# Optimization experiments

Hardware: AMD Instinct MI355X
Metric: run time of the kernel (lower is better)

## Reference

```python
import jax, jax.numpy as jnp
import numpy as np

HIDDEN = 512
HEADS = 8
DHEAD = HIDDEN // HEADS  # 64


def setup_inputs() -> dict:
    key = jax.random.key(0)
    ks = jax.random.split(key, 12)
    B, S = 2, 2048
    inp = {
        "q": jax.random.normal(ks[0], (B, S, HIDDEN), dtype=jnp.float32),
        "k": jax.random.normal(ks[1], (B, S, HIDDEN), dtype=jnp.float32),
        "v": jax.random.normal(ks[2], (B, S, HIDDEN), dtype=jnp.float32),
        "mask": jnp.zeros((B, 1, 1, S), dtype=bool),
    }
    scale = 1.0 / np.sqrt(HIDDEN)
    for i, name in enumerate(["Wq", "Wk", "Wv", "Wm"]):
        inp[name] = jax.random.normal(ks[3 + i], (HIDDEN, HIDDEN), dtype=jnp.float32) * scale
    for i, name in enumerate(["bq", "bk", "bv", "bm"]):
        inp[name] = jax.random.normal(ks[7 + i], (HIDDEN,), dtype=jnp.float32) * 0.01
    return inp


def reference(q, k, v, mask, Wq, Wk, Wv, Wm, bq, bk, bv, bm):
    B = q.shape[0]
    # Linear projections (torch Linear: x @ W.T + b)
    qh = (jnp.einsum("bsd,ed->bse", q, Wq) + bq).reshape(B, HEADS, -1, DHEAD)
    kh = (jnp.einsum("bsd,ed->bse", k, Wk) + bk).reshape(B, HEADS, -1, DHEAD)
    vh = (jnp.einsum("bsd,ed->bse", v, Wv) + bv).reshape(B, HEADS, -1, DHEAD)
    # NOTE: the original module reshapes [B,S,512] -> [B,8,S',64] directly
    # (splitting the sequence dim into heads, not the hidden dim); replicated here.
    s = jnp.einsum("bhqd,bhkd->bhqk", qh, kh) / jnp.sqrt(jnp.float32(DHEAD))
    s = jnp.where(mask, jnp.float32(-1e9), s)
    s = jax.nn.softmax(s, axis=-1)
    # dropout is identity in eval mode
    attn = jnp.einsum("bhqk,bhkd->bhqd", s, vh)  # [B,H,S',64]
    attn = attn.transpose(0, 2, 1, 3).reshape(B, -1, HIDDEN)
    return jnp.einsum("bsd,ed->bse", attn, Wm) + bm
```

## Files before the change

### kernel.cpp

```cpp
#include <hip/hip_runtime.h>
#include <hip/hip_bf16.h>
#include <math.h>

typedef float  f32x4 __attribute__((ext_vector_type(4)));
typedef short  s16x8 __attribute__((ext_vector_type(8)));
typedef short  s16x4 __attribute__((ext_vector_type(4)));
typedef unsigned short u16x4 __attribute__((ext_vector_type(4)));

__device__ inline unsigned short bfc(float f){
  __hip_bfloat16 h = __float2bfloat16(f);
  unsigned short u; __builtin_memcpy(&u, &h, 2); return u;
}

__device__ inline f32x4 mfma16(s16x4 a, s16x4 b, f32x4 c){
#if __has_builtin(__builtin_amdgcn_mfma_f32_16x16x16_bf16)
  return __builtin_amdgcn_mfma_f32_16x16x16_bf16(a, b, c, 0, 0, 0);
#elif __has_builtin(__builtin_amdgcn_mfma_f32_16x16x16bf16_1k)
  return __builtin_amdgcn_mfma_f32_16x16x16bf16_1k(a, b, c, 0, 0, 0);
#else
  asm("v_mfma_f32_16x16x16_bf16 %0, %1, %2, %0" : "+v"(c) : "v"(a), "v"(b));
  return c;
#endif
}

__device__ inline void gl_lds16(const unsigned short* g, unsigned short* l){
  __builtin_amdgcn_global_load_lds(
      (const __attribute__((address_space(1))) unsigned int*)g,
      (__attribute__((address_space(3))) unsigned int*)l, 16, 0, 0);
}

__global__ __launch_bounds__(256) void prep(const float* __restrict__ q, const float* __restrict__ k,
                                            const float* __restrict__ v,
                                            const float* __restrict__ w0, const float* __restrict__ w1,
                                            const float* __restrict__ w2, const float* __restrict__ w3,
                                            const unsigned char* __restrict__ mask,
                                            unsigned short* __restrict__ AP, unsigned short* __restrict__ WP,
                                            float* __restrict__ mf){
  int y = blockIdx.y;
  int t = blockIdx.x * 256 + threadIdx.x;
  if (y < 3){
    const float* src = y==0 ? q : (y==1 ? k : v);
    unsigned short* d = AP + (size_t)y * 2097152;
    int r = t >> 6, g = t & 63;
    const float* sp = src + (size_t)r * 512 + g * 8;
    f32x4 a0 = *(const f32x4*)sp;
    f32x4 a1 = *(const f32x4*)(sp + 4);
    s16x8 o = { (short)bfc(a0.x),(short)bfc(a0.y),(short)bfc(a0.z),(short)bfc(a0.w),
                (short)bfc(a1.x),(short)bfc(a1.y),(short)bfc(a1.z),(short)bfc(a1.w) };
    size_t off = ((size_t)(((r>>4)*16 + (g>>2))*64 + (g&3)*16 + (r&15))) * 8;
    *(s16x8*)(d + off) = o;
  } else if (y < 7){
    if (blockIdx.x < 128){
      int yy = y - 3;
      const float* src = yy==0 ? w0 : yy==1 ? w1 : yy==2 ? w2 : w3;
      int c = t >> 6, g = t & 63;
      const float* sp = src + (size_t)c * 512 + g * 8;
      f32x4 a0 = *(const f32x4*)sp;
      f32x4 a1 = *(const f32x4*)(sp + 4);
      s16x8 o = { (short)bfc(a0.x),(short)bfc(a0.y),(short)bfc(a0.z),(short)bfc(a0.w),
                  (short)bfc(a1.x),(short)bfc(a1.y),(short)bfc(a1.z),(short)bfc(a1.w) };
      size_t off = ((size_t)(((c>>4)*16 + (g>>2))*64 + (g&3)*16 + (c&15))) * 8;
      *(s16x8*)(WP + yy*262144 + off) = o;
    }
  } else if (t < 4096){
    mf[t] = mask[t] ? -1.442695e9f : 0.0f;
  }
}

__global__ __launch_bounds__(256) void proj_gemm(const unsigned short* __restrict__ Ap,
    const unsigned short* __restrict__ Wp,
    const float* __restrict__ bq, const float* __restrict__ bk, const float* __restrict__ bv,
    unsigned short* __restrict__ pout){
  int z = blockIdx.z;
  const unsigned short* A = Ap + (size_t)z * 2097152;
  const unsigned short* W = Wp + (size_t)z * 262144;
  const float* bias = z==0 ? bq : (z==1 ? bk : bv);
  unsigned short* out = pout + (size_t)z * 2097152;

  int w = threadIdx.x >> 6, lane = threadIdx.x & 63;
  int lr = lane & 15, lg = lane >> 4;
  int rt = blockIdx.x * 4 + w;
  int bn = blockIdx.y;

  f32x4 acc[4] = {};
  const unsigned short* Abase = A + ((size_t)rt*8192 + lane*8);
  const unsigned short* Wbase = W + ((size_t)bn*32768 + lane*8);
#pragma unroll 4
  for (int kc = 0; kc < 16; ++kc){
    s16x8 af = *(const s16x8*)(Abase + kc*512);
#pragma unroll
    for (int n = 0; n < 4; ++n){
      s16x8 bf = *(const s16x8*)(Wbase + ((size_t)n*16 + kc)*512);
      acc[n] = __builtin_amdgcn_mfma_f32_16x16x32_bf16(af, bf, acc[n], 0, 0, 0);
    }
  }
  int orow = rt*16 + lg*4;
#pragma unroll
  for (int n = 0; n < 4; ++n){
    int col = bn*64 + n*16 + lr;
    float bv_ = bias[col];
#pragma unroll
    for (int r = 0; r < 4; ++r)
      out[(size_t)(orow + r)*512 + col] = bfc(acc[n][r] + bv_);
  }
}

__global__ __launch_bounds__(256) void vtrans(const unsigned short* __restrict__ Pv,
                                              unsigned short* __restrict__ Vt){
  int kt = blockIdx.x, bh = blockIdx.y;
  int b = bh >> 3, h = bh & 7;
  __shared__ unsigned short t[64][65];
  const unsigned short* src = Pv + (size_t)(b*2048 + h*256)*512 + kt*4096;
  for (int i = threadIdx.x; i < 4096; i += 256){ int r = i >> 6, c = i & 63; t[r][c] = src[i]; }
  __syncthreads();
  unsigned short* dst = Vt + (size_t)bh*131072 + kt*64;
  for (int i = threadIdx.x; i < 4096; i += 256){ int d = i >> 6, kk = i & 63; dst[(size_t)d*2048 + kk] = t[kk][d]; }
}

__global__ __launch_bounds__(512, 4) void flash(const unsigned short* __restrict__ Pq,
                                             const unsigned short* __restrict__ Pk,
                                             const unsigned short* __restrict__ Vt,
                                             const float* __restrict__ mf,
                                             unsigned short* __restrict__ aout){
  int qt = blockIdx.x;
  int bh = blockIdx.y;
  int b = bh >> 3, h = bh & 7;
  int w = threadIdx.x >> 6;
  int wq = w & 1, wk = w >> 1;
  int lane = threadIdx.x & 63;
  int lr = lane & 15, lg = lane >> 4;

  const unsigned short* Qh  = Pq + (size_t)(b*2048 + h*256)*512;
  const unsigned short* Kh  = Pk + (size_t)(b*2048 + h*256)*512 + (size_t)wk*32768;
  const unsigned short* Vth = Vt + (size_t)bh*131072 + wk*512;
  const float* mp = mf + b*2048 + wk*512 + lg*4;

  __shared__ char smem[65536];
  unsigned short* ktile = (unsigned short*)smem;
  unsigned short* vtile = (unsigned short*)(smem + 32768);
  float* obuf = (float*)smem;
  float* mlb  = (float*)(smem + 49152);

  int krow_l = lane >> 3;
  int cxor  = (lane & 7) ^ krow_l;
  int kcol_l = cxor * 8;

  int vhalf32 = (cxor >> 2) * 32;
  int vkc = (cxor & 3) * 8;
  const unsigned short* kg0 = Kh + (size_t)(8*(wq*2+0) + krow_l)*64 + kcol_l;
  const unsigned short* kg1 = Kh + (size_t)(8*(wq*2+1) + krow_l)*64 + kcol_l;
  const unsigned short* vg0 = Vth + (size_t)(wq*16 + 0 + krow_l + vhalf32)*2048 + vkc;
  const unsigned short* vg1 = Vth + (size_t)(wq*16 + 8 + krow_l + vhalf32)*2048 + vkc;

  s16x8 qf[2][2];
#pragma unroll
  for (int qq = 0; qq < 2; ++qq){
    int qrow = qt*64 + wq*32 + qq*16 + lr;
    qf[qq][0] = *(const s16x8*)(Qh + (size_t)qrow*64 + lg*8);
    qf[qq][1] = *(const s16x8*)(Qh + (size_t)qrow*64 + 32 + lg*8);
  }

  float m2[2] = {-INFINITY, -INFINITY}, l[2] = {0.f, 0.f};
  f32x4 accT[2][4] = {};
  int kswz = (lr & 7) * 16;

#define STAGE(dbuf) { \
    unsigned short* kd = ktile + ((dbuf)*4 + wk)*2048; \
    unsigned short* vd = vtile + ((dbuf)*4 + wk)*2048; \
    gl_lds16(kg0, kd + (wq*2+0)*512); \
    gl_lds16(kg1, kd + (wq*2+1)*512); \
    gl_lds16(vg0, vd + (wq*2+0)*512); \
    gl_lds16(vg1, vd + (wq*2+1)*512); \
    kg0 += 2048; kg1 += 2048; vg0 += 32; vg1 += 32; }

  STAGE(0)
  __syncthreads();
  int cur = 0;

  for (int t = 0; t < 16; ++t){
    if (t < 15) STAGE(cur ^ 1)

    const char* kb = (const char*)(ktile + (cur*4 + wk)*2048);
    const char* vb = (const char*)(vtile + (cur*4 + wk)*2048);

    float s2[2][2][4];
    __builtin_amdgcn_s_setprio(1);
#pragma unroll
    for (int n = 0; n < 2; ++n){
      int krow = n*16 + lr;
      s16x8 kf0 = *(const s16x8*)(kb + krow*128 + ((lg*16) ^ kswz));
      s16x8 kf1 = *(const s16x8*)(kb + krow*128 + ((64 + lg*16) ^ kswz));
      f32x4 mv = *(const f32x4*)(mp + n*16);
#pragma unroll
      for (int qq = 0; qq < 2; ++qq){
        f32x4 a = {};
        a = __builtin_amdgcn_mfma_f32_16x16x32_bf16(kf0, qf[qq][0], a, 0, 0, 0);
        a = __builtin_amdgcn_mfma_f32_16x16x32_bf16(kf1, qf[qq][1], a, 0, 0, 0);
#pragma unroll
        for (int r = 0; r < 4; ++r)
          s2[qq][n][r] = __builtin_fmaf(a[r], 0.18033688f, mv[r]);
      }
    }
    __builtin_amdgcn_s_setprio(0);

    s16x4 pf[2][2];
#pragma unroll
    for (int qq = 0; qq < 2; ++qq){
      float t0 = fmaxf(fmaxf(s2[qq][0][0], s2[qq][0][1]), fmaxf(s2[qq][0][2], s2[qq][0][3]));
      float t1 = fmaxf(fmaxf(s2[qq][1][0], s2[qq][1][1]), fmaxf(s2[qq][1][2], s2[qq][1][3]));
      float rm = fmaxf(t0, t1);
      rm = fmaxf(rm, __shfl_xor(rm, 16));
      rm = fmaxf(rm, __shfl_xor(rm, 32));
      if (!__all(rm <= m2[qq] + 11.54f)){
        float mn = fmaxf(m2[qq], rm);
        float al = __builtin_amdgcn_exp2f(m2[qq] - mn);
        l[qq] *= al;
#pragma unroll
        for (int nd = 0; nd < 4; ++nd)
#pragma unroll
          for (int r = 0; r < 4; ++r) accT[qq][nd][r] *= al;
        m2[qq] = mn;
      }
#pragma unroll
      for (int n = 0; n < 2; ++n){
        float p0 = __builtin_amdgcn_exp2f(s2[qq][n][0] - m2[qq]);
        float p1 = __builtin_amdgcn_exp2f(s2[qq][n][1] - m2[qq]);
        float p2 = __builtin_amdgcn_exp2f(s2[qq][n][2] - m2[qq]);
        float p3 = __builtin_amdgcn_exp2f(s2[qq][n][3] - m2[qq]);
        l[qq] += (p0 + p1) + (p2 + p3);
        pf[qq][n] = (s16x4){ (short)bfc(p0), (short)bfc(p1), (short)bfc(p2), (short)bfc(p3) };
      }
    }

    __builtin_amdgcn_s_setprio(1);
#pragma unroll
    for (int n = 0; n < 2; ++n){
#pragma unroll
      for (int nd = 0; nd < 4; ++nd){
        int vrow = (nd & 1)*16 + lr;
        int vchunk = ((nd >> 1)*4 + n*2 + (lg >> 1)) ^ (vrow & 7);
        s16x4 vf = *(const s16x4*)(vb + vrow*128 + vchunk*16 + (lg & 1)*8);
        accT[0][nd] = mfma16(vf, pf[0][n], accT[0][nd]);
        accT[1][nd] = mfma16(vf, pf[1][n], accT[1][nd]);
      }
    }
    __builtin_amdgcn_s_setprio(0);

    mp += 32;
    __syncthreads();
    cur ^= 1;
  }
#undef STAGE

  float lt[2];
#pragma unroll
  for (int qq = 0; qq < 2; ++qq){
    float x = l[qq] + __shfl_xor(l[qq], 16);
    lt[qq] = x + __shfl_xor(x, 32);
  }

  if (wk != 0){
    int j = wk - 1;
#pragma unroll
    for (int qq = 0; qq < 2; ++qq){
      int reg = j*4 + wq*2 + qq;
      if (lg == 0){ mlb[reg*16 + lr] = m2[qq]; mlb[192 + reg*16 + lr] = lt[qq]; }
#pragma unroll
      for (int nd = 0; nd < 4; ++nd)
        *(f32x4*)&obuf[((size_t)reg*64 + lane)*16 + nd*4] = accT[qq][nd];
    }
  }
  __syncthreads();
  if (wk == 0){
#pragma unroll
    for (int qq = 0; qq < 2; ++qq){
      float mj[3], lj[3];
      float mM = m2[qq];
#pragma unroll
      for (int j = 0; j < 3; ++j){
        int reg = j*4 + wq*2 + qq;
        mj[j] = mlb[reg*16 + lr];
        lj[j] = mlb[192 + reg*16 + lr];
        mM = fmaxf(mM, mj[j]);
      }
      float a0 = __builtin_amdgcn_exp2f(m2[qq] - mM);
      float aj[3];
      float ltot = lt[qq] * a0;
#pragma unroll
      for (int j = 0; j < 3; ++j){
        aj[j] = __builtin_amdgcn_exp2f(mj[j] - mM);
        ltot += lj[j] * aj[j];
      }
      float inv = 1.f / ltot;
      int q = qt*64 + wq*32 + qq*16 + lr;
      int rt = (b*2048 + q) >> 4;
#pragma unroll
      for (int nd = 0; nd < 4; ++nd){
        f32x4 o = accT[qq][nd] * a0;
#pragma unroll
        for (int j = 0; j < 3; ++j){
          int reg = j*4 + wq*2 + qq;
          f32x4 oj = *(const f32x4*)&obuf[((size_t)reg*64 + lane)*16 + nd*4];
          o += oj * aj[j];
        }
        int g = h*8 + nd*2 + (lg >> 1);
        u16x4 ov = { bfc(o[0]*inv), bfc(o[1]*inv), bfc(o[2]*inv), bfc(o[3]*inv) };
        unsigned short* dp = aout + ((size_t)((rt*16 + (g>>2))*64 + (g&3)*16 + lr))*8 + (lg&1)*4;
        *(u16x4*)dp = ov;
      }
    }
  }
}

__global__ __launch_bounds__(256) void gemm_out(const unsigned short* __restrict__ Ap,
                                                const unsigned short* __restrict__ Wp,
                                                const float* __restrict__ bias,
                                                float* __restrict__ out){
  int w = threadIdx.x >> 6, lane = threadIdx.x & 63;
  int lr = lane & 15, lg = lane >> 4;
  int rt = blockIdx.x * 4 + w;
  int bn = blockIdx.y;
  f32x4 acc[4] = {};
  const unsigned short* Abase = Ap + ((size_t)rt*8192 + lane*8);
  const unsigned short* Wbase = Wp + ((size_t)bn*32768 + lane*8);
#pragma unroll 4
  for (int kc = 0; kc < 16; ++kc){
    s16x8 af = *(const s16x8*)(Abase + kc*512);
#pragma unroll
    for (int n = 0; n < 4; ++n){
      s16x8 bf = *(const s16x8*)(Wbase + ((size_t)n*16 + kc)*512);
      acc[n] = __builtin_amdgcn_mfma_f32_16x16x32_bf16(af, bf, acc[n], 0, 0, 0);
    }
  }
  int orow = rt*16 + lg*4;
#pragma unroll
  for (int n = 0; n < 4; ++n){
    int col = bn*64 + n*16 + lr;
    float bv_ = bias[col];
#pragma unroll
    for (int r = 0; r < 4; ++r)
      out[(size_t)(orow + r)*512 + col] = acc[n][r] + bv_;
  }
}

extern "C" void kernel_launch(void* const* d_in, const int* in_sizes, int n_in,
                              void* d_out, int out_size, void* d_ws, size_t ws_size,
                              hipStream_t stream) {
  const float* q  = (const float*)d_in[0];
  const float* k  = (const float*)d_in[1];
  const float* v  = (const float*)d_in[2];
  const unsigned char* mask = (const unsigned char*)d_in[3];
  const float* Wq = (const float*)d_in[4];
  const float* Wk = (const float*)d_in[5];
  const float* Wv = (const float*)d_in[6];
  const float* Wm = (const float*)d_in[7];
  const float* bq = (const float*)d_in[8];
  const float* bk = (const float*)d_in[9];
  const float* bv = (const float*)d_in[10];
  const float* bm = (const float*)d_in[11];

  unsigned short* ws = (unsigned short*)d_ws;
  unsigned short* WP   = ws;
  float*          MF   = (float*)(ws + 1048576);
  unsigned short* AP   = ws + 1056768;
  unsigned short* PQ   = ws + 7348224;
  unsigned short* VT   = ws + 13639680;
  unsigned short* AO   = ws + 15736832;

  prep<<<dim3(1024, 8), 256, 0, stream>>>(q, k, v, Wq, Wk, Wv, Wm, mask, AP, WP, MF);
  proj_gemm<<<dim3(64, 8, 3), 256, 0, stream>>>(AP, WP, bq, bk, bv, PQ);
  vtrans<<<dim3(32, 16), 256, 0, stream>>>(PQ + 2*2097152, VT);
  flash<<<dim3(32, 16), 512, 0, stream>>>(PQ, PQ + 2097152, VT, MF, AO);
  gemm_out<<<dim3(64, 8), 256, 0, stream>>>(AO, WP + 3*262144, bm, (float*)d_out);
}
```

Measured before the change: 82.29 us.

## Give each wave private double-buffered K/V tiles and drop per-iteration block barriers

Each wave now stages its own 16-key K and V slices into a private LDS region, instead of two waves cooperatively staging a shared 32-key tile. The loop runs 32 iterations of 16 keys and uses an explicit vmcnt wait in place of the per-iteration __syncthreads, with a single barrier added before the cross-wave merge that reuses the LDS. This is meant to remove block-wide barrier stalls. The cost is duplicated K/V global loads across the wq waves, and the final iteration's prefetch reads past the wave's key range.

```diff
diff --git a/kernel.cpp b/kernel.cpp
--- a/kernel.cpp
+++ b/kernel.cpp
@@ -133,24 +133,19 @@
   const unsigned short* Qh  = Pq + (size_t)(b*2048 + h*256)*512;
   const unsigned short* Kh  = Pk + (size_t)(b*2048 + h*256)*512 + (size_t)wk*32768;
   const unsigned short* Vth = Vt + (size_t)bh*131072 + wk*512;
-  const float* mp = mf + b*2048 + wk*512 + lg*4;
+  const float* mq = mf + b*2048 + wk*512 + lg*4;
 
   __shared__ char smem[65536];
-  unsigned short* ktile = (unsigned short*)smem;
-  unsigned short* vtile = (unsigned short*)(smem + 32768);
+  char* wbase = smem + w*8192;
   float* obuf = (float*)smem;
   float* mlb  = (float*)(smem + 49152);
 
-  int krow_l = lane >> 3;
-  int cxor  = (lane & 7) ^ krow_l;
-  int kcol_l = cxor * 8;
-
-  int vhalf32 = (cxor >> 2) * 32;
-  int vkc = (cxor & 3) * 8;
-  const unsigned short* kg0 = Kh + (size_t)(8*(wq*2+0) + krow_l)*64 + kcol_l;
-  const unsigned short* kg1 = Kh + (size_t)(8*(wq*2+1) + krow_l)*64 + kcol_l;
-  const unsigned short* vg0 = Vth + (size_t)(wq*16 + 0 + krow_l + vhalf32)*2048 + vkc;
-  const unsigned short* vg1 = Vth + (size_t)(wq*16 + 8 + krow_l + vhalf32)*2048 + vkc;
+  int row_l = lane >> 3;
+  int jp = (lane & 7) ^ row_l;
+  const unsigned short* kg0 = Kh + (size_t)row_l*64 + jp*8;
+  const unsigned short* kg1 = kg0 + 512;
+  const unsigned short* vg0 = Vth + (size_t)(row_l + 16*(jp>>1))*2048 + (jp&1)*8;
+  const unsigned short* vg1 = vg0 + 8*2048;
 
   s16x8 qf[2][2];
 #pragma unroll
@@ -165,50 +160,44 @@
   int kswz = (lr & 7) * 16;
 
 #define STAGE(dbuf) { \
-    unsigned short* kd = ktile + ((dbuf)*4 + wk)*2048; \
-    unsigned short* vd = vtile + ((dbuf)*4 + wk)*2048; \
-    gl_lds16(kg0, kd + (wq*2+0)*512); \
-    gl_lds16(kg1, kd + (wq*2+1)*512); \
-    gl_lds16(vg0, vd + (wq*2+0)*512); \
-    gl_lds16(vg1, vd + (wq*2+1)*512); \
-    kg0 += 2048; kg1 += 2048; vg0 += 32; vg1 += 32; }
+    unsigned short* kd = (unsigned short*)(wbase + (dbuf)*2048); \
+    unsigned short* vd = (unsigned short*)(wbase + 4096 + (dbuf)*2048); \
+    gl_lds16(kg0, kd); gl_lds16(kg1, kd + 512); \
+    gl_lds16(vg0, vd); gl_lds16(vg1, vd + 512); \
+    kg0 += 1024; kg1 += 1024; vg0 += 16; vg1 += 16; }
 
   STAGE(0)
-  __syncthreads();
   int cur = 0;
 
-  for (int t = 0; t < 16; ++t){
-    if (t < 15) STAGE(cur ^ 1)
-
-    const char* kb = (const char*)(ktile + (cur*4 + wk)*2048);
-    const char* vb = (const char*)(vtile + (cur*4 + wk)*2048);
-
-    float s2[2][2][4];
+#pragma unroll 2
+  for (int t = 0; t < 32; ++t){
+    STAGE(cur ^ 1)
+    asm volatile("s_waitcnt vmcnt(4)" ::: "memory");
+    __builtin_amdgcn_sched_barrier(0);
+
+    const char* kb = wbase + cur*2048;
+    const char* vb = wbase + 4096 + cur*2048;
+
+    s16x8 kf0 = *(const s16x8*)(kb + lr*128 + ((lg*16) ^ kswz));
+    s16x8 kf1 = *(const s16x8*)(kb + lr*128 + ((64 + lg*16) ^ kswz));
+    f32x4 mv = *(const f32x4*)(mq + t*16);
+    float s2[2][4];
     __builtin_amdgcn_s_setprio(1);
 #pragma unroll
-    for (int n = 0; n < 2; ++n){
-      int krow = n*16 + lr;
-      s16x8 kf0 = *(const s16x8*)(kb + krow*128 + ((lg*16) ^ kswz));
-      s16x8 kf1 = *(const s16x8*)(kb + krow*128 + ((64 + lg*16) ^ kswz));
-      f32x4 mv = *(const f32x4*)(mp + n*16);
-#pragma unroll
-      for (int qq = 0; qq < 2; ++qq){
-        f32x4 a = {};
-        a = __builtin_amdgcn_mfma_f32_16x16x32_bf16(kf0, qf[qq][0], a, 0, 0, 0);
-        a = __builtin_amdgcn_mfma_f32_16x16x32_bf16(kf1, qf[qq][1], a, 0, 0, 0);
-#pragma unroll
-        for (int r = 0; r < 4; ++r)
-          s2[qq][n][r] = __builtin_fmaf(a[r], 0.18033688f, mv[r]);
-      }
+    for (int qq = 0; qq < 2; ++qq){
+      f32x4 a = {};
+      a = __builtin_amdgcn_mfma_f32_16x16x32_bf16(kf0, qf[qq][0], a, 0, 0, 0);
+      a = __builtin_amdgcn_mfma_f32_16x16x32_bf16(kf1, qf[qq][1], a, 0, 0, 0);
+#pragma unroll
+      for (int r = 0; r < 4; ++r)
+        s2[qq][r] = __builtin_fmaf(a[r], 0.18033688f, mv[r]);
     }
     __builtin_amdgcn_s_setprio(0);
 
-    s16x4 pf[2][2];
+    s16x4 pf[2];
 #pragma unroll
     for (int qq = 0; qq < 2; ++qq){
-      float t0 = fmaxf(fmaxf(s2[qq][0][0], s2[qq][0][1]), fmaxf(s2[qq][0][2], s2[qq][0][3]));
-      float t1 = fmaxf(fmaxf(s2[qq][1][0], s2[qq][1][1]), fmaxf(s2[qq][1][2], s2[qq][1][3]));
-      float rm = fmaxf(t0, t1);
+      float rm = fmaxf(fmaxf(s2[qq][0], s2[qq][1]), fmaxf(s2[qq][2], s2[qq][3]));
       rm = fmaxf(rm, __shfl_xor(rm, 16));
       rm = fmaxf(rm, __shfl_xor(rm, 32));
       if (!__all(rm <= m2[qq] + 11.54f)){
@@ -221,33 +210,24 @@
           for (int r = 0; r < 4; ++r) accT[qq][nd][r] *= al;
         m2[qq] = mn;
       }
-#pragma unroll
-      for (int n = 0; n < 2; ++n){
-        float p0 = __builtin_amdgcn_exp2f(s2[qq][n][0] - m2[qq]);
-        float p1 = __builtin_amdgcn_exp2f(s2[qq][n][1] - m2[qq]);
-        float p2 = __builtin_amdgcn_exp2f(s2[qq][n][2] - m2[qq]);
-        float p3 = __builtin_amdgcn_exp2f(s2[qq][n][3] - m2[qq]);
-        l[qq] += (p0 + p1) + (p2 + p3);
-        pf[qq][n] = (s16x4){ (short)bfc(p0), (short)bfc(p1), (short)bfc(p2), (short)bfc(p3) };
-      }
+      float p0 = __builtin_amdgcn_exp2f(s2[qq][0] - m2[qq]);
+      float p1 = __builtin_amdgcn_exp2f(s2[qq][1] - m2[qq]);
+      float p2 = __builtin_amdgcn_exp2f(s2[qq][2] - m2[qq]);
+      float p3 = __builtin_amdgcn_exp2f(s2[qq][3] - m2[qq]);
+      l[qq] += (p0 + p1) + (p2 + p3);
+      pf[qq] = (s16x4){ (short)bfc(p0), (short)bfc(p1), (short)bfc(p2), (short)bfc(p3) };
     }
 
     __builtin_amdgcn_s_setprio(1);
 #pragma unroll
-    for (int n = 0; n < 2; ++n){
-#pragma unroll
-      for (int nd = 0; nd < 4; ++nd){
-        int vrow = (nd & 1)*16 + lr;
-        int vchunk = ((nd >> 1)*4 + n*2 + (lg >> 1)) ^ (vrow & 7);
-        s16x4 vf = *(const s16x4*)(vb + vrow*128 + vchunk*16 + (lg & 1)*8);
-        accT[0][nd] = mfma16(vf, pf[0][n], accT[0][nd]);
-        accT[1][nd] = mfma16(vf, pf[1][n], accT[1][nd]);
-      }
+    for (int nd = 0; nd < 4; ++nd){
+      int j = (nd*2 + (lg >> 1)) ^ (lr & 7);
+      s16x4 vf = *(const s16x4*)(vb + lr*128 + j*16 + (lg & 1)*8);
+      accT[0][nd] = mfma16(vf, pf[0], accT[0][nd]);
+      accT[1][nd] = mfma16(vf, pf[1], accT[1][nd]);
     }
     __builtin_amdgcn_s_setprio(0);
 
-    mp += 32;
-    __syncthreads();
     cur ^= 1;
   }
 #undef STAGE
@@ -258,6 +238,8 @@
     float x = l[qq] + __shfl_xor(l[qq], 16);
     lt[qq] = x + __shfl_xor(x, 32);
   }
+
+  __syncthreads();
 
   if (wk != 0){
     int j = wk - 1;
```

Measured after the change: 91.28 us. +10.9%, slower.
